# Kernel tuning notes

Measured on AMD Instinct MI355X. Metric: run time of the kernel, lower is better.

Reference implementation:

```python
import math
import jax, jax.numpy as jnp
import numpy as np

B, T, E = 2, 2048, 2048
NUM_HEADS = 16
H = NUM_HEADS // 2          # differential head pairs = 8
D = E // NUM_HEADS          # head_dim = 128
DEPTH = 12
LAMBDA_INIT = 0.8 - 0.6 * math.exp(-0.3 * DEPTH)
EPS = 1e-5


def setup_inputs() -> dict:
    key = jax.random.key(0)
    ks = jax.random.split(key, 10)
    sc = lambda k, shape, std: jax.random.normal(k, shape, dtype=jnp.float32) * std
    return {
        "x": jax.random.normal(ks[0], (B, T, E), dtype=jnp.float32),
        "Wq": sc(ks[1], (E, E), 0.02),   # [in, out]
        "Wk": sc(ks[2], (E, E), 0.02),   # n_rep == 1 -> k/v proj width = embed_dim
        "Wv": sc(ks[3], (E, E), 0.02),
        "Wo": sc(ks[4], (E, E), 0.02),
        "lambda_q1": sc(ks[5], (D,), 0.1),
        "lambda_k1": sc(ks[6], (D,), 0.1),
        "lambda_q2": sc(ks[7], (D,), 0.1),
        "lambda_k2": sc(ks[8], (D,), 0.1),
        "g": jnp.ones((2 * D,), dtype=jnp.float32),  # RMSNorm weight
    }


def _forward(x, Wq, Wk, Wv, Wo, lq1, lk1, lq2, lk2, g):
    Bz, Tl, _ = x.shape
    # projections; view(bsz, T, 2*H, D).reshape(bsz, T, H, 2, D): adjacent head
    # pairs become the two differential components.
    q = (x @ Wq).reshape(Bz, Tl, H, 2, D)
    k = (x @ Wk).reshape(Bz, Tl, H, 2, D)
    v = (x @ Wv).reshape(Bz, Tl, H, 2 * D)   # value width is 2*head_dim

    scale = D ** -0.5                         # SDPA default scaling
    causal = jnp.tril(jnp.ones((Tl, Tl), dtype=bool))  # is_causal=True

    def attend(qc, kc):
        # qc, kc: [B, T, H, D]
        s = jnp.einsum('bthd,bshd->bhts', qc, kc) * scale
        s = jnp.where(causal, s, -jnp.inf)
        a = jax.nn.softmax(s, axis=-1)
        return jnp.einsum('bhts,bshe->bthe', a, v)  # [B, T, H, 2D]

    # interleaved q/k + repeated v in the single SDPA == two attention maps on full V
    o1 = attend(q[..., 0, :], k[..., 0, :])
    o2 = attend(q[..., 1, :], k[..., 1, :])

    lam = jnp.exp(jnp.sum(lq1 * lk1)) - jnp.exp(jnp.sum(lq2 * lk2)) + LAMBDA_INIT
    o = o1 - lam * o2
    # RMSNorm over last dim (2*head_dim), eps=1e-5, learned weight g
    o = o * jax.lax.rsqrt(jnp.mean(o * o, axis=-1, keepdims=True) + EPS) * g
    o = o * (1.0 - LAMBDA_INIT)
    return o.reshape(Bz, Tl, E) @ Wo


def reference(x, Wq, Wk, Wv, Wo, lambda_q1, lambda_k1, lambda_q2, lambda_k2, g):
    return _forward(x, Wq, Wk, Wv, Wo, lambda_q1, lambda_k1, lambda_q2, lambda_k2, g)
```

## Files before the change

### kernel.cpp

```cpp
#include <hip/hip_runtime.h>
#include <stdint.h>
#include <math.h>


typedef unsigned short u16;
typedef short bf16x8 __attribute__((ext_vector_type(8)));
typedef float f32x4 __attribute__((ext_vector_type(4)));

typedef uint32_t __attribute__((address_space(1))) as1_u32;
typedef uint32_t __attribute__((address_space(3))) as3_u32;

#define LAMBDA_INIT 0.78360576653162453f

__device__ __forceinline__ u16 f2bf(float f) {
  uint32_t u = __float_as_uint(f);
  u += 0x7FFFu + ((u >> 16) & 1u);
  return (u16)(u >> 16);
}
__device__ __forceinline__ float bf2f(u16 v) {
  return __uint_as_float(((uint32_t)v) << 16);
}

__device__ __forceinline__ void async16(u16* lds, const u16* g) {
  __builtin_amdgcn_global_load_lds((const as1_u32*)(uintptr_t)g,
                                   (as3_u32*)(uint32_t)(uintptr_t)lds, 16, 0, 0);
}

__device__ __forceinline__ f32x4 mfma16(bf16x8 a, bf16x8 b, f32x4 c) {
  return __builtin_amdgcn_mfma_f32_16x16x32_bf16(a, b, c, 0, 0, 0);
}


__global__ void cast_x_kernel(const float* __restrict__ x, u16* __restrict__ xb, int n4) {
  int i = blockIdx.x * 256 + threadIdx.x;
  if (i < n4) {
    float4 v = ((const float4*)x)[i];
    ushort4 o;
    o.x = f2bf(v.x); o.y = f2bf(v.y); o.z = f2bf(v.z); o.w = f2bf(v.w);
    ((ushort4*)xb)[i] = o;
  }
}

__global__ void transpose_w4_kernel(const float* __restrict__ W0, const float* __restrict__ W1,
                                    const float* __restrict__ W2, const float* __restrict__ W3,
                                    u16* __restrict__ Wt4) {
  __shared__ float tile[32][33];
  int z = blockIdx.z;
  const float* W = (z == 0) ? W0 : (z == 1) ? W1 : (z == 2) ? W2 : W3;
  u16* Wt = Wt4 + (size_t)z * 4194304;
  int tx = threadIdx.x, ty = threadIdx.y;
  int c0 = blockIdx.x * 32, r0 = blockIdx.y * 32;
#pragma unroll
  for (int i = 0; i < 32; i += 8)
    tile[ty + i][tx] = W[(size_t)(r0 + ty + i) * 2048 + c0 + tx];
  __syncthreads();
#pragma unroll
  for (int i = 0; i < 32; i += 8)
    Wt[(size_t)(c0 + ty + i) * 2048 + r0 + tx] = f2bf(tile[tx][ty + i]);
}

__global__ void lam_kernel(const float* __restrict__ lq1, const float* __restrict__ lk1,
                           const float* __restrict__ lq2, const float* __restrict__ lk2,
                           float* __restrict__ out) {
  int L = threadIdx.x;
  float d1 = lq1[L] * lk1[L] + lq1[L + 64] * lk1[L + 64];
  float d2 = lq2[L] * lk2[L] + lq2[L + 64] * lk2[L + 64];
#pragma unroll
  for (int m = 1; m < 64; m <<= 1) {
    d1 += __shfl_xor(d1, m);
    d2 += __shfl_xor(d2, m);
  }
  if (L == 0) out[0] = __expf(d1) - __expf(d2) + LAMBDA_INIT;
}


__device__ __forceinline__ void stage256(const u16* base, int K, int k0, u16* lds, int t_) {
#pragma unroll
  for (int i = 0; i < 2; i++) {
    int s = t_ + i * 512;
    int row = s >> 2, gp = s & 3;
    int gs = gp ^ ((row >> 1) & 3);
    async16(&lds[s * 8], base + (size_t)row * K + k0 + gs * 8);
  }
}

__global__ __launch_bounds__(512, 2) void gemm256_kernel(const u16* __restrict__ A,
                                                         const u16* __restrict__ Bt,
                                                         u16* __restrict__ Cout,
                                                         int M, int N, int K) {
  __shared__ __attribute__((aligned(16))) u16 Ls[4][2][256 * 32];
  int t_ = threadIdx.x;
  int lane = t_ & 63, w = t_ >> 6;
  int lr = lane & 15, lq = lane >> 4;
  int m0 = blockIdx.y * 256, n0 = blockIdx.x * 256;
  int wm = (w >> 2) * 128, wn = (w & 3) * 64;
  const u16* Ab = A + (size_t)m0 * K;
  const u16* Bb = Bt + (size_t)n0 * K;
  int NT = K >> 5;
  f32x4 acc[8][4] = {};

#pragma unroll
  for (int p = 0; p < 3; p++) {
    stage256(Ab, K, p * 32, &Ls[p][0][0], t_);
    stage256(Bb, K, p * 32, &Ls[p][1][0], t_);
  }
  asm volatile("s_waitcnt vmcnt(8)" ::: "memory");
  __builtin_amdgcn_s_barrier();
  __builtin_amdgcn_sched_barrier(0);

#pragma unroll 1
  for (int t = 0; t < NT; t++) {
    int d = t & 3;
    const u16* As_ = &Ls[d][0][0];
    const u16* Bs_ = &Ls[d][1][0];
    bool stg = (t + 3 < NT);
    int k0n = (t + 3) * 32;
    int dn = (t + 3) & 3;

    bf16x8 b4[4], a0[4];
#pragma unroll
    for (int nf = 0; nf < 4; nf++) {
      int rb = wn + nf * 16 + lr;
      b4[nf] = *(const bf16x8*)&Bs_[rb * 32 + (lq ^ ((rb >> 1) & 3)) * 8];
    }
#pragma unroll
    for (int mf = 0; mf < 4; mf++) {
      int ra = wm + mf * 16 + lr;
      a0[mf] = *(const bf16x8*)&As_[ra * 32 + (lq ^ ((ra >> 1) & 3)) * 8];
    }
    if (stg) stage256(Ab, K, k0n, &Ls[dn][0][0], t_);
    __builtin_amdgcn_s_setprio(1);
#pragma unroll
    for (int mf = 0; mf < 4; mf++)
#pragma unroll
      for (int nf = 0; nf < 4; nf++)
        acc[mf][nf] = mfma16(a0[mf], b4[nf], acc[mf][nf]);
    __builtin_amdgcn_s_setprio(0);

    bf16x8 a1[4];
#pragma unroll
    for (int mf = 0; mf < 4; mf++) {
      int ra = wm + 64 + mf * 16 + lr;
      a1[mf] = *(const bf16x8*)&As_[ra * 32 + (lq ^ ((ra >> 1) & 3)) * 8];
    }
    if (stg) stage256(Bb, K, k0n, &Ls[dn][1][0], t_);
    __builtin_amdgcn_s_setprio(1);
#pragma unroll
    for (int mf = 0; mf < 4; mf++)
#pragma unroll
      for (int nf = 0; nf < 4; nf++)
        acc[4 + mf][nf] = mfma16(a1[mf], b4[nf], acc[4 + mf][nf]);
    __builtin_amdgcn_s_setprio(0);

    if (t < NT - 3)      asm volatile("s_waitcnt vmcnt(8)" ::: "memory");
    else if (t < NT - 2) asm volatile("s_waitcnt vmcnt(4)" ::: "memory");
    else                 asm volatile("s_waitcnt vmcnt(0)" ::: "memory");
    __builtin_amdgcn_s_barrier();
    __builtin_amdgcn_sched_barrier(0);
  }

#pragma unroll
  for (int mf = 0; mf < 8; mf++)
#pragma unroll
    for (int nf = 0; nf < 4; nf++)
#pragma unroll
      for (int r = 0; r < 4; r++) {
        int row = m0 + wm + mf * 16 + lq * 4 + r;
        int col = n0 + wn + nf * 16 + lr;
        Cout[(size_t)row * N + col] = f2bf(acc[mf][nf][r]);
      }
}

template <int OUT_BF16>
__global__ __launch_bounds__(256, 3) void gemm_bt_kernel(const u16* __restrict__ A,
                                                         const u16* __restrict__ Bt,
                                                         void* __restrict__ Cout,
                                                         int M, int N, int K) {
  __shared__ __attribute__((aligned(16))) u16 As[128 * 64];
  __shared__ __attribute__((aligned(16))) u16 Bs[128 * 64];
  int t = threadIdx.x;
  int lane = t & 63, w = t >> 6;
  int lr = lane & 15, lq = lane >> 4;
  int m0 = blockIdx.y * 128, n0 = blockIdx.x * 128;
  int wm = (w >> 1) * 64, wn = (w & 1) * 64;
  const u16* Ab = A + (size_t)m0 * K;
  const u16* Bb = Bt + (size_t)n0 * K;
  f32x4 acc[4][4] = {};

  for (int k0 = 0; k0 < K; k0 += 64) {
    __syncthreads();
#pragma unroll
    for (int i = 0; i < 4; i++) {
      int q = t + i * 256;
      int row = q >> 3, gp = q & 7;
      int gg = gp ^ (row & 7);
      async16(&As[q * 8], Ab + (size_t)row * K + k0 + gg * 8);
      async16(&Bs[q * 8], Bb + (size_t)row * K + k0 + gg * 8);
    }
    __syncthreads();
#pragma unroll
    for (int kk = 0; kk < 2; kk++) {
      bf16x8 a[4], b[4];
#pragma unroll
      for (int mi = 0; mi < 4; mi++) {
        int ra = wm + mi * 16 + lr;
        int rb = wn + mi * 16 + lr;
        a[mi] = *(const bf16x8*)&As[ra * 64 + ((kk * 4 + lq) ^ (ra & 7)) * 8];
        b[mi] = *(const bf16x8*)&Bs[rb * 64 + ((kk * 4 + lq) ^ (rb & 7)) * 8];
      }
#pragma unroll
      for (int mi = 0; mi < 4; mi++)
#pragma unroll
        for (int ni = 0; ni < 4; ni++)
          acc[mi][ni] = mfma16(a[mi], b[ni], acc[mi][ni]);
    }
  }
#pragma unroll
  for (int mi = 0; mi < 4; mi++) {
#pragma unroll
    for (int ni = 0; ni < 4; ni++) {
#pragma unroll
      for (int r = 0; r < 4; r++) {
        int row = m0 + wm + mi * 16 + lq * 4 + r;
        int col = n0 + wn + ni * 16 + lr;
        if (OUT_BF16)
          ((u16*)Cout)[(size_t)row * N + col] = f2bf(acc[mi][ni][r]);
        else
          ((float*)Cout)[(size_t)row * N + col] = acc[mi][ni][r];
      }
    }
  }
}


struct FlashCtx {
  const u16* Qbase;
  const u16* Kbase;
  const u16* Vbase;
  int t, w, lr, lq;
};

__device__ __forceinline__ void stage_k(const FlashCtx& cx, int jc, u16* Kn) {
#pragma unroll
  for (int i = 0; i < 4; i++) {
    int q = cx.t + i * 256;
    int row = q >> 4, gp = q & 15;
    int gg = (gp & 8) | ((gp & 7) ^ (row & 7));
    async16(&Kn[q * 8], cx.Kbase + (size_t)(jc + row) * 4096 + gg * 8);
  }
}

__device__ __forceinline__ void stage_v(const FlashCtx& cx, int jc, u16* Vs) {
#pragma unroll
  for (int i = 0; i < 8; i++) {
    int q = cx.t + i * 256;
    int e = q >> 3, gp = q & 7;
    int gg = gp ^ (e & 7);
    async16(&Vs[q * 8], cx.Vbase + (size_t)e * 4096 + jc + gg * 8);
  }
}

__global__ __launch_bounds__(256, 2) void flash_diff_kernel(const u16* __restrict__ QKb,
                                                            const u16* __restrict__ Vt,
                                                            u16* __restrict__ o12b) {
  __shared__ __attribute__((aligned(16))) u16 Ks0[64 * 128];
  __shared__ __attribute__((aligned(16))) u16 Ks1[64 * 128];
  __shared__ __attribute__((aligned(16))) u16 Vs[256 * 64];
  __shared__ __attribute__((aligned(16))) u16 Ps[4][16 * 88];

  int t = threadIdx.x;
  FlashCtx cx;
  cx.t = t; cx.w = t >> 6;
  cx.lr = t & 15; cx.lq = (t >> 4) & 3;

  int idx = blockIdx.x;
  int xcd = idx & 7, slot = idx >> 3;
  int pairI = slot & 15, ghi = slot >> 4;
  int g = ghi * 8 + xcd;
  int bh = g >> 1, c = g & 1;
  int b = bh >> 3, h = bh & 7;

  cx.Qbase = QKb + (size_t)b * 2048 * 4096 + h * 256 + c * 128;
  cx.Kbase = cx.Qbase + 2048;
  cx.Vbase = Vt + (size_t)(h * 256) * 4096 + b * 2048;
  u16* Op = o12b + (size_t)c * (4096ull * 2048) + (size_t)b * 2048 * 2048 + h * 256;
  u16* PsW = Ps[cx.w];

  u16* Kc = Ks0;
  u16* Kn = Ks1;

  stage_k(cx, 0, Kc);

#pragma unroll 1
  for (int phase = 0; phase < 2; phase++) {
    int qi = phase ? (31 - pairI) : pairI;
    int q0 = qi * 64;
    int nst = qi + 1;

    bf16x8 qa[4];
#pragma unroll
    for (int ks = 0; ks < 4; ks++)
      qa[ks] = *(const bf16x8*)&cx.Qbase[(size_t)(q0 + cx.w * 16 + cx.lr) * 4096 +
                                         ks * 32 + cx.lq * 8];

    f32x4 acc[16] = {};
    f32x4 lacc = {};
    float m_ = -INFINITY;
    int rowmax = q0 + cx.w * 16 + 15;

#pragma unroll 1
    for (int j = 0; j < nst; j++) {
      int jc = j * 64;
      int njc = (j + 1 < nst) ? (j + 1) * 64 : (phase == 0 ? 0 : -1);

      __syncthreads();
      stage_v(cx, jc, Vs);
      if (njc >= 0) stage_k(cx, njc, Kn);

      bool act = (jc <= rowmax);
      if (act) {
        f32x4 sacc[4] = {};
#pragma unroll
        for (int ks = 0; ks < 4; ks++) {
#pragma unroll
          for (int ni = 0; ni < 4; ni++) {
            int row = ni * 16 + cx.lr;
            int gk = ks * 4 + cx.lq;
            int gp = (gk & 8) | ((gk & 7) ^ (row & 7));
            bf16x8 kb = *(const bf16x8*)&Kc[row * 128 + gp * 8];
            sacc[ni] = mfma16(qa[ks], kb, sacc[ni]);
          }
        }

        const float k2 = 0.12753257550036097f;
        float s2[4][4];
        bool diag = (jc + 63 > q0 + cx.w * 16);
#pragma unroll
        for (int ni = 0; ni < 4; ni++)
#pragma unroll
          for (int r = 0; r < 4; r++) {
            float v = sacc[ni][r] * k2;
            if (diag) {
              int colg = jc + ni * 16 + cx.lr;
              int rowg = q0 + cx.w * 16 + cx.lq * 4 + r;
              if (colg > rowg) v = -INFINITY;
            }
            s2[ni][r] = v;
          }

        float sm = fmaxf(
            fmaxf(fmaxf(fmaxf(s2[0][0], s2[0][1]), fmaxf(s2[0][2], s2[0][3])),
                  fmaxf(fmaxf(s2[1][0], s2[1][1]), fmaxf(s2[1][2], s2[1][3]))),
            fmaxf(fmaxf(fmaxf(s2[2][0], s2[2][1]), fmaxf(s2[2][2], s2[2][3])),
                  fmaxf(fmaxf(s2[3][0], s2[3][1]), fmaxf(s2[3][2], s2[3][3]))));
        float mo = m_;
        if (__any(sm > mo + 8.0f)) {
          float mv = sm;
          mv = fmaxf(mv, __shfl_xor(mv, 1));
          mv = fmaxf(mv, __shfl_xor(mv, 2));
          mv = fmaxf(mv, __shfl_xor(mv, 4));
          mv = fmaxf(mv, __shfl_xor(mv, 8));
          mv = fmaxf(mv, __shfl_xor(mv, 16));
          mv = fmaxf(mv, __shfl_xor(mv, 32));
          float mn = fmaxf(mo, mv);
          float a = __builtin_amdgcn_exp2f(mo - mn);
#pragma unroll
          for (int ei = 0; ei < 16; ei++)
#pragma unroll
            for (int r = 0; r < 4; r++) acc[ei][r] *= a;
#pragma unroll
          for (int r = 0; r < 4; r++) lacc[r] *= a;
          m_ = mn;
          mo = mn;
        }

#pragma unroll
        for (int ni = 0; ni < 4; ni++)
#pragma unroll
          for (int r = 0; r < 4; r++) {
            float p = __builtin_amdgcn_exp2f(s2[ni][r] - mo);
            PsW[(cx.lq * 4 + r) * 88 + ni * 16 + cx.lr] =
                (u16)(__float_as_uint(p) >> 16);
          }
      }

      if (njc >= 0) asm volatile("s_waitcnt vmcnt(4)" ::: "memory");
      else          asm volatile("s_waitcnt vmcnt(0)" ::: "memory");
      __builtin_amdgcn_s_barrier();
      __builtin_amdgcn_sched_barrier(0);

      if (act) {
        const bf16x8 onesb = {0x3F80, 0x3F80, 0x3F80, 0x3F80,
                              0x3F80, 0x3F80, 0x3F80, 0x3F80};
        bf16x8 pa0 = *(const bf16x8*)&PsW[cx.lr * 88 + cx.lq * 8];
        bf16x8 pa1 = *(const bf16x8*)&PsW[cx.lr * 88 + 32 + cx.lq * 8];
        __builtin_amdgcn_s_setprio(1);
#pragma unroll
        for (int ei = 0; ei < 16; ei++) {
          int e = ei * 16 + cx.lr;
          int g0 = cx.lq ^ (e & 7);
          int g1 = g0 ^ 4;
          bf16x8 vb0 = *(const bf16x8*)&Vs[e * 64 + g0 * 8];
          bf16x8 vb1 = *(const bf16x8*)&Vs[e * 64 + g1 * 8];
          acc[ei] = mfma16(pa0, vb0, acc[ei]);
          acc[ei] = mfma16(pa1, vb1, acc[ei]);
        }
        lacc = mfma16(pa0, onesb, lacc);
        lacc = mfma16(pa1, onesb, lacc);
        __builtin_amdgcn_s_setprio(0);
      }

      u16* tmp = Kc; Kc = Kn; Kn = tmp;
    }

#pragma unroll
    for (int r = 0; r < 4; r++) {
      float inv = 1.0f / lacc[r];
      int row = q0 + cx.w * 16 + cx.lq * 4 + r;
#pragma unroll
      for (int ei = 0; ei < 16; ei++)
        Op[(size_t)row * 2048 + ei * 16 + cx.lr] = f2bf(acc[ei][r] * inv);
    }
  }
}

__global__ void combine_kernel(const u16* __restrict__ o12b, const float* __restrict__ lamp,
                               const float* __restrict__ g, u16* __restrict__ ob) {
  __shared__ float red[4];
  int t = threadIdx.x;
  int grp = blockIdx.x;
  size_t idx = (size_t)grp * 256 + t;
  const size_t comp = 4096ull * 2048;
  float lam = lamp[0];
  float v = bf2f(o12b[idx]) - lam * bf2f(o12b[idx + comp]);
  float ss = v * v;
  ss += __shfl_xor(ss, 1);
  ss += __shfl_xor(ss, 2);
  ss += __shfl_xor(ss, 4);
  ss += __shfl_xor(ss, 8);
  ss += __shfl_xor(ss, 16);
  ss += __shfl_xor(ss, 32);
  if ((t & 63) == 0) red[t >> 6] = ss;
  __syncthreads();
  float tot = red[0] + red[1] + red[2] + red[3];
  float scale = rsqrtf(tot * (1.0f / 256.0f) + 1e-5f) * (1.0f - LAMBDA_INIT);
  ob[(size_t)(grp >> 3) * 2048 + (grp & 7) * 256 + t] = f2bf(v * scale * g[t]);
}


extern "C" void kernel_launch(void* const* d_in, const int* in_sizes, int n_in,
                              void* d_out, int out_size, void* d_ws, size_t ws_size,
                              hipStream_t stream) {
  const float* x   = (const float*)d_in[0];
  const float* Wq  = (const float*)d_in[1];
  const float* Wk  = (const float*)d_in[2];
  const float* Wv  = (const float*)d_in[3];
  const float* Wo  = (const float*)d_in[4];
  const float* lq1 = (const float*)d_in[5];
  const float* lk1 = (const float*)d_in[6];
  const float* lq2 = (const float*)d_in[7];
  const float* lk2 = (const float*)d_in[8];
  const float* g   = (const float*)d_in[9];

  char* ws = (char*)d_ws;
  u16* xb    = (u16*)(ws);
  u16* Wtq   = (u16*)(ws + 16777216);
  u16* Wtv   = (u16*)(ws + 33554432);
  u16* Wto   = (u16*)(ws + 41943040);
  u16* QKb   = (u16*)(ws + 50331648);
  u16* Vt    = (u16*)(ws + 83886080);
  u16* o12b  = (u16*)(ws + 100663296);
  u16* ob    = (u16*)(ws + 134217728);
  float* lamp = (float*)(ws + 150994944);

  cast_x_kernel<<<8192, 256, 0, stream>>>(x, xb, 2097152);
  transpose_w4_kernel<<<dim3(64, 64, 4), dim3(32, 8), 0, stream>>>(Wq, Wk, Wv, Wo, Wtq);
  lam_kernel<<<1, 64, 0, stream>>>(lq1, lk1, lq2, lk2, lamp);

  gemm256_kernel<<<dim3(16, 16), 512, 0, stream>>>(xb, Wtq, QKb, 4096, 4096, 2048);
  gemm_bt_kernel<1><<<dim3(32, 16), 256, 0, stream>>>(Wtv, xb, Vt, 2048, 4096, 2048);

  flash_diff_kernel<<<512, 256, 0, stream>>>(QKb, Vt, o12b);
  combine_kernel<<<32768, 256, 0, stream>>>(o12b, lamp, g, ob);
  gemm_bt_kernel<0><<<dim3(16, 32), 256, 0, stream>>>(ob, Wto, (float*)d_out, 4096, 2048, 2048);
}
```

Baseline: 398.3 us.

## Replace V/output GEMMs with triple-buffered 128x256 tile kernel; reorder flash staging

The two smaller GEMMs (V projection and output projection) now use a new 512-thread kernel with 128x256 tiles, a K-step of 32, and a three-deep asynchronous LDS buffer ring with vmcnt-based waits instead of full syncthreads. This overlaps global loads with MFMA work and raises per-block compute. In the flash kernel, K staging is issued before V staging, and the manual partial vmcnt wait is replaced by a full __syncthreads, which waits for all outstanding loads including the prefetched K. That could reduce load/compute overlap in attention.

Result: no change. 402.1 us (+0.9%).

```diff
diff --git a/kernel.cpp b/kernel.cpp
--- a/kernel.cpp
+++ b/kernel.cpp
@@ -171,65 +171,103 @@
       }
 }
 
+
+__device__ __forceinline__ void stageA2(const u16* base, int K, int k0, u16* lds, int t_) {
+  int row = t_ >> 2, gp = t_ & 3;
+  int gs = gp ^ ((row >> 1) & 3);
+  async16(&lds[t_ * 8], base + (size_t)row * K + k0 + gs * 8);
+}
+__device__ __forceinline__ void stageB2(const u16* base, int K, int k0, u16* lds, int t_) {
+#pragma unroll
+  for (int i = 0; i < 2; i++) {
+    int s = t_ + i * 512;
+    int row = s >> 2, gp = s & 3;
+    int gs = gp ^ ((row >> 1) & 3);
+    async16(&lds[s * 8], base + (size_t)row * K + k0 + gs * 8);
+  }
+}
+
 template <int OUT_BF16>
-__global__ __launch_bounds__(256, 3) void gemm_bt_kernel(const u16* __restrict__ A,
-                                                         const u16* __restrict__ Bt,
-                                                         void* __restrict__ Cout,
-                                                         int M, int N, int K) {
-  __shared__ __attribute__((aligned(16))) u16 As[128 * 64];
-  __shared__ __attribute__((aligned(16))) u16 Bs[128 * 64];
-  int t = threadIdx.x;
-  int lane = t & 63, w = t >> 6;
+__global__ __launch_bounds__(512, 4) void gemm_bt2_kernel(const u16* __restrict__ A,
+                                                          const u16* __restrict__ Bt,
+                                                          void* __restrict__ Cout,
+                                                          int M, int N, int K) {
+  __shared__ __attribute__((aligned(16))) u16 LsA[3][128 * 32];
+  __shared__ __attribute__((aligned(16))) u16 LsB[3][256 * 32];
+  int t_ = threadIdx.x;
+  int lane = t_ & 63, w = t_ >> 6;
   int lr = lane & 15, lq = lane >> 4;
-  int m0 = blockIdx.y * 128, n0 = blockIdx.x * 128;
-  int wm = (w >> 1) * 64, wn = (w & 1) * 64;
+  int m0 = blockIdx.y * 128, n0 = blockIdx.x * 256;
+  int wm = (w >> 2) * 64, wn = (w & 3) * 64;
   const u16* Ab = A + (size_t)m0 * K;
   const u16* Bb = Bt + (size_t)n0 * K;
+  int NT = K >> 5;
   f32x4 acc[4][4] = {};
 
-  for (int k0 = 0; k0 < K; k0 += 64) {
-    __syncthreads();
-#pragma unroll
-    for (int i = 0; i < 4; i++) {
-      int q = t + i * 256;
-      int row = q >> 3, gp = q & 7;
-      int gg = gp ^ (row & 7);
-      async16(&As[q * 8], Ab + (size_t)row * K + k0 + gg * 8);
-      async16(&Bs[q * 8], Bb + (size_t)row * K + k0 + gg * 8);
-    }
-    __syncthreads();
-#pragma unroll
-    for (int kk = 0; kk < 2; kk++) {
-      bf16x8 a[4], b[4];
-#pragma unroll
-      for (int mi = 0; mi < 4; mi++) {
-        int ra = wm + mi * 16 + lr;
-        int rb = wn + mi * 16 + lr;
-        a[mi] = *(const bf16x8*)&As[ra * 64 + ((kk * 4 + lq) ^ (ra & 7)) * 8];
-        b[mi] = *(const bf16x8*)&Bs[rb * 64 + ((kk * 4 + lq) ^ (rb & 7)) * 8];
+#pragma unroll
+  for (int p = 0; p < 2; p++) {
+    stageA2(Ab, K, p * 32, &LsA[p][0], t_);
+    stageB2(Bb, K, p * 32, &LsB[p][0], t_);
+  }
+  asm volatile("s_waitcnt vmcnt(3)" ::: "memory");
+  __builtin_amdgcn_s_barrier();
+  __builtin_amdgcn_sched_barrier(0);
+
+  int d = 0, dn = 2;
+#pragma unroll 1
+  for (int t = 0; t < NT; t++) {
+    const u16* As_ = &LsA[d][0];
+    const u16* Bs_ = &LsB[d][0];
+    bool stg = (t + 2 < NT);
+    if (stg) {
+      int k0n = (t + 2) * 32;
+      stageA2(Ab, K, k0n, &LsA[dn][0], t_);
+      stageB2(Bb, K, k0n, &LsB[dn][0], t_);
+    }
+
+    bf16x8 a[4], b[4];
+#pragma unroll
+    for (int mf = 0; mf < 4; mf++) {
+      int ra = wm + mf * 16 + lr;
+      a[mf] = *(const bf16x8*)&As_[ra * 32 + (lq ^ ((ra >> 1) & 3)) * 8];
+    }
+#pragma unroll
+    for (int nf = 0; nf < 4; nf++) {
+      int rb = wn + nf * 16 + lr;
+      b[nf] = *(const bf16x8*)&Bs_[rb * 32 + (lq ^ ((rb >> 1) & 3)) * 8];
+    }
+    __builtin_amdgcn_s_setprio(1);
+#pragma unroll
+    for (int mf = 0; mf < 4; mf++)
+#pragma unroll
+      for (int nf = 0; nf < 4; nf++)
+        acc[mf][nf] = mfma16(a[mf], b[nf], acc[mf][nf]);
+    __builtin_amdgcn_s_setprio(0);
+
+    if (t < NT - 1) {
+      if (stg) asm volatile("s_waitcnt vmcnt(3)" ::: "memory");
+      else     asm volatile("s_waitcnt vmcnt(0)" ::: "memory");
+      __builtin_amdgcn_s_barrier();
+      __builtin_amdgcn_sched_barrier(0);
+    }
+
+    d = (d == 2) ? 0 : d + 1;
+    dn = (dn == 2) ? 0 : dn + 1;
+  }
+
+#pragma unroll
+  for (int mf = 0; mf < 4; mf++)
+#pragma unroll
+    for (int nf = 0; nf < 4; nf++)
+#pragma unroll
+      for (int r = 0; r < 4; r++) {
+        int row = m0 + wm + mf * 16 + lq * 4 + r;
+        int col = n0 + wn + nf * 16 + lr;
+        if (OUT_BF16)
+          ((u16*)Cout)[(size_t)row * N + col] = f2bf(acc[mf][nf][r]);
+        else
+          ((float*)Cout)[(size_t)row * N + col] = acc[mf][nf][r];
       }
-#pragma unroll
-      for (int mi = 0; mi < 4; mi++)
-#pragma unroll
-        for (int ni = 0; ni < 4; ni++)
-          acc[mi][ni] = mfma16(a[mi], b[ni], acc[mi][ni]);
-    }
-  }
-#pragma unroll
-  for (int mi = 0; mi < 4; mi++) {
-#pragma unroll
-    for (int ni = 0; ni < 4; ni++) {
-#pragma unroll
-      for (int r = 0; r < 4; r++) {
-        int row = m0 + wm + mi * 16 + lq * 4 + r;
-        int col = n0 + wn + ni * 16 + lr;
-        if (OUT_BF16)
-          ((u16*)Cout)[(size_t)row * N + col] = f2bf(acc[mi][ni][r]);
-        else
-          ((float*)Cout)[(size_t)row * N + col] = acc[mi][ni][r];
-      }
-    }
-  }
 }
 
 
@@ -314,8 +352,8 @@
       int njc = (j + 1 < nst) ? (j + 1) * 64 : (phase == 0 ? 0 : -1);
 
       __syncthreads();
+      if (njc >= 0) stage_k(cx, njc, Kn);
       stage_v(cx, jc, Vs);
-      if (njc >= 0) stage_k(cx, njc, Kn);
 
       bool act = (jc <= rowmax);
       if (act) {
@@ -384,11 +422,7 @@
           }
       }
 
-      if (njc >= 0) asm volatile("s_waitcnt vmcnt(4)" ::: "memory");
-      else          asm volatile("s_waitcnt vmcnt(0)" ::: "memory");
-      __builtin_amdgcn_s_barrier();
-      __builtin_amdgcn_sched_barrier(0);
-
+      __syncthreads();
       if (act) {
         const bf16x8 onesb = {0x3F80, 0x3F80, 0x3F80, 0x3F80,
                               0x3F80, 0x3F80, 0x3F80, 0x3F80};
@@ -478,9 +512,9 @@
   lam_kernel<<<1, 64, 0, stream>>>(lq1, lk1, lq2, lk2, lamp);
 
   gemm256_kernel<<<dim3(16, 16), 512, 0, stream>>>(xb, Wtq, QKb, 4096, 4096, 2048);
-  gemm_bt_kernel<1><<<dim3(32, 16), 256, 0, stream>>>(Wtv, xb, Vt, 2048, 4096, 2048);
+  gemm_bt2_kernel<1><<<dim3(16, 16), 512, 0, stream>>>(Wtv, xb, Vt, 2048, 4096, 2048);
 
   flash_diff_kernel<<<512, 256, 0, stream>>>(QKb, Vt, o12b);
   combine_kernel<<<32768, 256, 0, stream>>>(o12b, lamp, g, ob);
-  gemm_bt_kernel<0><<<dim3(16, 32), 256, 0, stream>>>(ob, Wto, (float*)d_out, 4096, 2048, 2048);
-}
+  gemm_bt2_kernel<0><<<dim3(8, 32), 512, 0, stream>>>(ob, Wto, (float*)d_out, 4096, 2048, 2048);
+}
```
